# Performance work log

Hardware: AMD Instinct MI355X
Metric: run time of the kernel (lower is better)

The kernel has to match this reference:

```python
import jax, jax.numpy as jnp
import numpy as np

B, S, W = 128, 100, 20
D, L, H, DFF = 192, 6, 8, 256
DH = D // H

def _ln(x, g, b, eps=1e-5):
    m = jnp.mean(x, -1, keepdims=True)
    v = jnp.var(x, -1, keepdims=True)
    return (x - m) * jax.lax.rsqrt(v + eps) * g + b

def _pos_encoding(seq_len, d):
    pos = np.arange(seq_len, dtype=np.float32)[:, None]
    div = np.exp(np.arange(0, d, 2, dtype=np.float32) * (-np.log(10000.0) / d))
    pe = np.zeros((seq_len, d), dtype=np.float32)
    pe[:, 0::2] = np.sin(pos * div)
    pe[:, 1::2] = np.cos(pos * div)
    return jnp.asarray(pe)

def setup_inputs() -> dict:
    key = jax.random.key(0)
    ks = iter(jax.random.split(key, 80))
    def nrm(shape, s=0.05):
        return jax.random.normal(next(ks), shape, jnp.float32) * s
    inp = {
        'title_idx': jax.random.randint(next(ks), (B, S, W), 0, 1000),
        'class_idx': jax.random.randint(next(ks), (B, S, W), 0, 500),
        'process_idx': jax.random.randint(next(ks), (B, S, W), 0, 1000),
        'activity_type': jax.random.randint(next(ks), (B, S), 0, 4),
        'mouse_pos': jax.random.uniform(next(ks), (B, S, 2), jnp.float32),
        'rect': jax.random.uniform(next(ks), (B, S, W, 4), jnp.float32),
        'flags': jax.random.uniform(next(ks), (B, S, W, 2), jnp.float32),
        'keyboard_active': jax.random.uniform(next(ks), (B, S, 1), jnp.float32),
        'window_mask': jnp.ones((B, S, W), jnp.float32),
        'noise': jax.random.normal(next(ks), (W, B, D), jnp.float32),
        'title_emb': nrm((1000, 32)),
        'class_emb': nrm((500, 32)),
        'process_emb': nrm((1000, 32)),
        'spatial_w1': nrm((64, 6)), 'spatial_b1': nrm((64,)),
        'spatial_w2': nrm((32, 64)), 'spatial_b2': nrm((32,)),
        'wfuse_w': nrm((128, 128)), 'wfuse_b': nrm((128,)),
        'mouse_w1': nrm((32, 2)), 'mouse_b1': nrm((32,)),
        'mouse_w2': nrm((32, 32)), 'mouse_b2': nrm((32,)),
        'act_emb': nrm((4, 16)),
        'kbd_w': nrm((16, 1)), 'kbd_b': nrm((16,)),
        'afuse_w': nrm((64, 64)), 'afuse_b': nrm((64,)),
        'qkv_w': nrm((L, 3 * D, D)), 'qkv_b': nrm((L, 3 * D)),
        'out_w': nrm((L, D, D)), 'out_b': nrm((L, D)),
        'ff1_w': nrm((L, DFF, D)), 'ff1_b': nrm((L, DFF)),
        'ff2_w': nrm((L, D, DFF)), 'ff2_b': nrm((L, D)),
        'ln1_g': 1.0 + nrm((L, D)), 'ln1_b': nrm((L, D)),
        'ln2_g': 1.0 + nrm((L, D)), 'ln2_b': nrm((L, D)),
        'proj_w1': nrm((256, 192)), 'proj_b1': nrm((256,)),
        'proj_w2': nrm((4, 256)), 'proj_b2': nrm((4,)),
        'ex_w1': nrm((128, 192)), 'ex_b1': nrm((128,)),
        'ex_w2': nrm((1, 128)), 'ex_b2': nrm((1,)),
    }
    return inp

def reference(title_idx, class_idx, process_idx, activity_type, mouse_pos, rect, flags, keyboard_active, window_mask, noise, title_emb, class_emb, process_emb, spatial_w1, spatial_b1, spatial_w2, spatial_b2, wfuse_w, wfuse_b, mouse_w1, mouse_b1, mouse_w2, mouse_b2, act_emb, kbd_w, kbd_b, afuse_w, afuse_b, qkv_w, qkv_b, out_w, out_b, ff1_w, ff1_b, ff2_w, ff2_b, ln1_g, ln1_b, ln2_g, ln2_b, proj_w1, proj_b1, proj_w2, proj_b2, ex_w1, ex_b1, ex_w2, ex_b2):
    # ---- window feature extraction (vectorized over B,S,W) ----
    t = title_emb[title_idx]              # [B,S,W,32]
    c = class_emb[class_idx]
    p = process_emb[process_idx]
    sp_in = jnp.concatenate([rect, flags], -1)  # [B,S,W,6]
    sp = jax.nn.relu(sp_in @ spatial_w1.T + spatial_b1) @ spatial_w2.T + spatial_b2
    wcomb = jnp.concatenate([t, c, p, sp], -1)  # [B,S,W,128]
    wf = jax.nn.relu(wcomb @ wfuse_w.T + wfuse_b) * window_mask[..., None]
    avg_w = jnp.sum(wf, 2) / W            # mean over max_windows incl zero padding
    # ---- activity feature extraction ----
    mp = mouse_pos / jnp.array([1920.0, 1080.0], jnp.float32)
    mf = jax.nn.relu(mp @ mouse_w1.T + mouse_b1) @ mouse_w2.T + mouse_b2  # [B,S,32]
    ae = act_emb[activity_type]           # [B,S,16]
    kf = keyboard_active @ kbd_w.T + kbd_b  # [B,S,16]
    af = jax.nn.relu(jnp.concatenate([mf, ae, kf], -1) @ afuse_w.T + afuse_b)
    # ---- transformer ----
    x = jnp.concatenate([avg_w, af], -1) + _pos_encoding(S, D)[None]  # [B,S,192]
    scale = 1.0 / np.sqrt(DH)
    def block(h, prm):
        qw, qb, ow, ob, f1w, f1b, f2w, f2b, g1, b1, g2, b2 = prm
        qkv = h @ qw.T + qb
        q, k, v = jnp.split(qkv, 3, -1)
        q = q.reshape(B, S, H, DH); k = k.reshape(B, S, H, DH); v = v.reshape(B, S, H, DH)
        a = jax.nn.softmax(jnp.einsum('bqhd,bkhd->bhqk', q, k) * scale, -1)
        o = jnp.einsum('bhqk,bkhd->bqhd', a, v).reshape(B, S, D)
        h = _ln(h + o @ ow.T + ob, g1, b1)
        ff = jax.nn.relu(h @ f1w.T + f1b) @ f2w.T + f2b
        return _ln(h + ff, g2, b2), None
    x, _ = jax.lax.scan(block, x, (qkv_w, qkv_b, out_w, out_b, ff1_w, ff1_b, ff2_w, ff2_b, ln1_g, ln1_b, ln2_g, ln2_b))
    last = x[:, -1, :]                    # [B,192]
    # ---- per-slot heads (noise passed in deterministically) ----
    slot = last[None] + noise * 0.1       # [W,B,192]
    positions = jnp.transpose(jax.nn.relu(slot @ proj_w1.T + proj_b1) @ proj_w2.T + proj_b2, (1, 0, 2))  # [B,W,4]
    existence = jnp.transpose(jax.nn.sigmoid(jax.nn.relu(slot @ ex_w1.T + ex_b1) @ ex_w2.T + ex_b2)[..., 0], (1, 0))  # [B,W]
    return positions, existence
```

## Files before the change

### kernel.cpp

```cpp
#include <hip/hip_runtime.h>
#include <hip/hip_bf16.h>
#include <math.h>

#define B_ 128
#define S_ 100
#define W_ 20
#define D_ 192
#define L_ 6
#define H_ 8
#define DFF_ 256
#define DH_ 24
#define BS_ (B_*S_)
#define THREED_ 576

typedef short short8 __attribute__((ext_vector_type(8)));
typedef short short4v __attribute__((ext_vector_type(4)));
typedef float floatx16 __attribute__((ext_vector_type(16)));

__device__ __forceinline__ float posenc(int s, int c) {
  float freq = expf(-logf(10000.f) * (float)(2 * (c >> 1)) / (float)D_);
  float ang = (float)s * freq;
  return (c & 1) ? cosf(ang) : sinf(ang);
}

__device__ __forceinline__ short8 ld_frag8(const __hip_bfloat16* p) {
  short4v lo = *(const short4v*)p;
  short4v hi = *(const short4v*)(p + 4);
  short8 r;
  r[0]=lo[0]; r[1]=lo[1]; r[2]=lo[2]; r[3]=lo[3];
  r[4]=hi[0]; r[5]=hi[1]; r[6]=hi[2]; r[7]=hi[3];
  return r;
}

__device__ __forceinline__ short f2bf_s(float v) {
  __hip_bfloat16 t = __float2bfloat16(v);
  return *reinterpret_cast<short*>(&t);
}

__global__ __launch_bounds__(256)
void convertprep_kernel(
    const float* __restrict__ s0, __hip_bfloat16* __restrict__ d0,
    const float* __restrict__ s1, __hip_bfloat16* __restrict__ d1,
    const float* __restrict__ s2, __hip_bfloat16* __restrict__ d2,
    const float* __restrict__ s3, __hip_bfloat16* __restrict__ d3,
    const float* __restrict__ te, const float* __restrict__ ce,
    const float* __restrict__ pe, const float* __restrict__ wfw,
    const float* __restrict__ wfb, const float* __restrict__ sw2,
    const float* __restrict__ sb2,
    float* __restrict__ TE2, float* __restrict__ CE2,
    float* __restrict__ PE2, __hip_bfloat16* __restrict__ WSPb)
{
  int b = blockIdx.x, tid = threadIdx.x;
  if (b < 720) {
    const float* s; __hip_bfloat16* d; int base;
    if      (b < 324) { s = s0; d = d0; base = b; }
    else if (b < 432) { s = s1; d = d1; base = b - 324; }
    else if (b < 576) { s = s2; d = d2; base = b - 432; }
    else              { s = s3; d = d3; base = b - 576; }
    int i = (base * 256 + tid) * 8;
    float4 v0 = *(const float4*)(s + i);
    float4 v1 = *(const float4*)(s + i + 4);
    __hip_bfloat162* d2p = (__hip_bfloat162*)(d + i);
    d2p[0] = __float22bfloat162_rn(make_float2(v0.x, v0.y));
    d2p[1] = __float22bfloat162_rn(make_float2(v0.z, v0.w));
    d2p[2] = __float22bfloat162_rn(make_float2(v1.x, v1.y));
    d2p[3] = __float22bfloat162_rn(make_float2(v1.z, v1.w));
    return;
  }
  int blk = b - 720;
  if (blk < 1250) {
    int item = blk * 256 + tid;
    int v = item >> 7, o = item & 127;
    const float* src; float* dst; int base, vv;
    float a;
    if (v < 1000) {
      src = te; dst = TE2; base = 0; vv = v;
      a = wfb[o];
      #pragma unroll 8
      for (int k = 0; k < 32; ++k) a += wfw[o * 128 + 96 + k] * sb2[k];
    } else if (v < 1500) {
      src = ce; dst = CE2; base = 32; vv = v - 1000; a = 0.f;
    } else {
      src = pe; dst = PE2; base = 64; vv = v - 1500; a = 0.f;
    }
    #pragma unroll 8
    for (int k = 0; k < 32; ++k) a += src[vv * 32 + k] * wfw[o * 128 + base + k];
    dst[vv * 128 + o] = a;
  } else {
    int item = (blk - 1250) * 256 + tid;
    int j = item >> 7, o = item & 127;
    float a = 0.f;
    #pragma unroll 8
    for (int k = 0; k < 32; ++k) a += wfw[o * 128 + 96 + k] * sw2[k * 64 + j];
    WSPb[o * 64 + j] = __float2bfloat16(a);
  }
}

__global__ __launch_bounds__(256)
void encode8_kernel(
    const int* __restrict__ title_idx, const int* __restrict__ class_idx,
    const int* __restrict__ process_idx, const int* __restrict__ activity_type,
    const float* __restrict__ mouse_pos, const float* __restrict__ rect,
    const float* __restrict__ flags, const float* __restrict__ keyboard_active,
    const float* __restrict__ window_mask,
    const float* __restrict__ sw1, const float* __restrict__ sb1,
    const float* __restrict__ TE2, const float* __restrict__ CE2,
    const float* __restrict__ PE2, const __hip_bfloat16* __restrict__ WSPb,
    const float* __restrict__ mw1, const float* __restrict__ mb1,
    const float* __restrict__ mw2, const float* __restrict__ mb2,
    const float* __restrict__ act_emb, const float* __restrict__ kbw,
    const float* __restrict__ kbb,
    const float* __restrict__ afw, const float* __restrict__ afb,
    float* __restrict__ x, __hip_bfloat16* __restrict__ xb)
{
  __shared__ __hip_bfloat16 Bls[128][72];
  __shared__ int   idxS[4][20][3];
  __shared__ float maskS[4][20];
  __shared__ __align__(16) char aux[2560];
  float (*rectS)[20][8] = (float(*)[20][8])aux;
  float (*afA)[68]      = (float(*)[68])aux;
  float (*afB)[68]      = (float(*)[68])(aux + 1088);

  int tid = threadIdx.x;
  int w = tid >> 6, lane = tid & 63;
  int m32 = lane & 31, half = lane >> 5;
  int bs0 = blockIdx.x * 4;
  int bs = bs0 + w;

  for (int e = tid; e < 240; e += 256) {
    int g2 = e / 60, rem = e % 60, which = rem / 20, w_ = rem % 20;
    const int* src = (which == 0) ? title_idx : (which == 1) ? class_idx : process_idx;
    idxS[g2][w_][which] = src[(bs0 + g2) * W_ + w_];
  }
  if (tid < 80) {
    int g2 = tid / 20, w_ = tid % 20;
    maskS[g2][w_] = window_mask[(bs0 + g2) * W_ + w_];
  }
  for (int e = tid; e < 480; e += 256) {
    int g2 = e / 120, rem = e % 120, w_ = rem / 6, c = rem % 6;
    int rg = (bs0 + g2) * W_ + w_;
    rectS[g2][w_][c] = (c < 4) ? rect[rg * 4 + c] : flags[rg * 2 + (c - 4)];
  }
  for (int e = tid; e < 1024; e += 256) {
    int col = e >> 3, k8 = e & 7;
    short8 v = *(const short8*)&WSPb[col * 64 + k8 * 8];
    *(short8*)&Bls[col][k8 * 8] = v;
  }
  __syncthreads();

  short8 afr[4];
  {
    float rc[6];
    bool act = (m32 < W_);
    if (act) {
      #pragma unroll
      for (int c = 0; c < 6; ++c) rc[c] = rectS[w][m32][c];
    }
    #pragma unroll
    for (int s = 0; s < 4; ++s) {
      short8 f;
      #pragma unroll
      for (int jp = 0; jp < 8; ++jp) {
        float a = 0.f;
        if (act) {
          int j = s * 16 + half * 8 + jp;
          const float* w1 = sw1 + j * 6;
          a = sb1[j];
          #pragma unroll
          for (int c = 0; c < 6; ++c) a += w1[c] * rc[c];
          a = fmaxf(a, 0.f);
        }
        f[jp] = f2bf_s(a);
      }
      afr[s] = f;
    }
  }

  floatx16 acc[4];
  #pragma unroll
  for (int nt = 0; nt < 4; ++nt)
    #pragma unroll
    for (int r = 0; r < 16; ++r) acc[nt][r] = 0.f;

  #pragma unroll
  for (int s = 0; s < 4; ++s) {
    int ko = s * 16 + half * 8;
    #pragma unroll
    for (int nt = 0; nt < 4; ++nt) {
      short8 bf = *(const short8*)&Bls[nt * 32 + m32][ko];
      acc[nt] = __builtin_amdgcn_mfma_f32_32x32x16_bf16(afr[s], bf, acc[nt], 0, 0, 0);
    }
  }

  float cs[4] = {0.f, 0.f, 0.f, 0.f};
  #pragma unroll
  for (int r = 0; r < 16; ++r) {
    int row = (r & 3) + 8 * (r >> 2) + 4 * half;
    if (row < W_) {
      int t  = idxS[w][row][0];
      int ci = idxS[w][row][1];
      int p  = idxS[w][row][2];
      float mk = maskS[w][row];
      #pragma unroll
      for (int nt = 0; nt < 4; ++nt) {
        int col = nt * 32 + m32;
        float gs = TE2[(size_t)t  * 128 + col]
                 + CE2[(size_t)ci * 128 + col]
                 + PE2[(size_t)p  * 128 + col];
        cs[nt] += fmaxf(acc[nt][r] + gs, 0.f) * mk;
      }
    }
  }
  #pragma unroll
  for (int nt = 0; nt < 4; ++nt) cs[nt] += __shfl_xor(cs[nt], 32);
  if (half == 0) {
    int s_ = bs % S_;
    #pragma unroll
    for (int nt = 0; nt < 4; ++nt) {
      int col = nt * 32 + m32;
      float v = cs[nt] * (1.f / (float)W_) + posenc(s_, col);
      x[(size_t)bs * D_ + col] = v;
      xb[(size_t)bs * D_ + col] = __float2bfloat16(v);
    }
  }

  int bl = tid >> 6, ln63 = tid & 63;
  int bsg = bs0 + bl;
  __syncthreads();
  if (ln63 < 32) {
    float mx = mouse_pos[bsg * 2 + 0] * (1.f / 1920.f);
    float my = mouse_pos[bsg * 2 + 1] * (1.f / 1080.f);
    afA[bl][ln63] = fmaxf(mw1[ln63 * 2] * mx + mw1[ln63 * 2 + 1] * my + mb1[ln63], 0.f);
  }
  __syncthreads();
  float cv;
  if (ln63 < 32) {
    float a = mb2[ln63];
    #pragma unroll 8
    for (int k = 0; k < 32; ++k) a += mw2[ln63 * 32 + k] * afA[bl][k];
    cv = a;
  } else if (ln63 < 48) {
    cv = act_emb[activity_type[bsg] * 16 + (ln63 - 32)];
  } else {
    cv = kbw[ln63 - 48] * keyboard_active[bsg] + kbb[ln63 - 48];
  }
  __syncthreads();
  afB[bl][ln63] = cv;
  __syncthreads();
  {
    float a = afb[ln63];
    const float4* w4 = (const float4*)(afw + ln63 * 64);
    const float4* cp = (const float4*)&afB[bl][0];
    #pragma unroll
    for (int k4 = 0; k4 < 16; ++k4) {
      float4 ww = w4[k4], c2 = cp[k4];
      a += ww.x*c2.x + ww.y*c2.y + ww.z*c2.z + ww.w*c2.w;
    }
    float v = fmaxf(a, 0.f);
    int cg = 128 + ln63;
    float ovv = v + posenc(bsg % S_, cg);
    x[(size_t)bsg * D_ + cg] = ovv;
    xb[(size_t)bsg * D_ + cg] = __float2bfloat16(ovv);
  }
}

__global__ __launch_bounds__(256)
void qkvattn_kernel(const __hip_bfloat16* __restrict__ xb,
                    const __hip_bfloat16* __restrict__ Wq,
                    const float* __restrict__ qb,
                    __hip_bfloat16* __restrict__ o)
{
  __shared__ __align__(16) char smem[40960];
  __hip_bfloat16* Asl = (__hip_bfloat16*)smem;
  __hip_bfloat16* Bsl = (__hip_bfloat16*)(smem + 10240);
  __hip_bfloat16* Qs  = (__hip_bfloat16*)smem;
  __hip_bfloat16* Ks  = (__hip_bfloat16*)(smem + 10240);
  __hip_bfloat16* Ps  = (__hip_bfloat16*)smem;
  __hip_bfloat16* Vt  = (__hip_bfloat16*)(smem + 33792);

  int bh = blockIdx.x;
  int hh = bh & 7, b = bh >> 3;
  int tid = threadIdx.x, lane = tid & 63, w = tid >> 6;
  int m32 = lane & 31, half = lane >> 5;

  for (int e = tid; e < (32 * 112) / 8; e += 256)
    ((float4*)Vt)[e] = make_float4(0.f, 0.f, 0.f, 0.f);

  int rA = tid >> 1, hA = tid & 1;
  int rrA = rA < S_ ? rA : S_ - 1;
  size_t baseA = (size_t)(b * S_ + rrA) * D_;
  float4* dA = (float4*)&Asl[rA * 40 + hA * 16];

  bool isB = (tid < 192);
  int rB = tid >> 1;
  int tB = rB >> 5, jB = rB & 31;
  bool actB = isB && (jB < DH_);
  size_t baseB = actB ? (size_t)(tB * D_ + hh * DH_ + jB) * D_ : 0;
  float4* dB = (float4*)&Bsl[rB * 40 + hA * 16];

  if (isB && !actB) {
    float4 z = make_float4(0.f, 0.f, 0.f, 0.f);
    dB[0] = z; dB[1] = z;
  }
  {
    float4 a0, a1, b0, b1;
    const float4* s = (const float4*)&xb[baseA + hA * 16];
    a0 = s[0]; a1 = s[1];
    if (actB) {
      const float4* sB = (const float4*)&Wq[baseB + hA * 16];
      b0 = sB[0]; b1 = sB[1];
      dB[0] = b0; dB[1] = b1;
    }
    dA[0] = a0; dA[1] = a1;
  }

  floatx16 acc[3];
  #pragma unroll
  for (int t = 0; t < 3; ++t)
    #pragma unroll
    for (int r = 0; r < 16; ++r) acc[t][r] = 0.f;

  for (int k0 = 0; k0 < D_; k0 += 32) {
    bool more = (k0 + 32 < D_);
    __syncthreads();
    float4 na0, na1, nb0, nb1;
    if (more) {
      const float4* s = (const float4*)&xb[baseA + k0 + 32 + hA * 16];
      na0 = s[0]; na1 = s[1];
      if (actB) {
        const float4* sB = (const float4*)&Wq[baseB + k0 + 32 + hA * 16];
        nb0 = sB[0]; nb1 = sB[1];
      }
    }
    #pragma unroll
    for (int kc = 0; kc < 2; ++kc) {
      int ko = kc * 16 + half * 8;
      short8 a = *(const short8*)&Asl[(w * 32 + m32) * 40 + ko];
      #pragma unroll
      for (int t = 0; t < 3; ++t) {
        short8 bf = *(const short8*)&Bsl[(t * 32 + m32) * 40 + ko];
        acc[t] = __builtin_amdgcn_mfma_f32_32x32x16_bf16(a, bf, acc[t], 0, 0, 0);
      }
    }
    __syncthreads();
    if (more) {
      dA[0] = na0; dA[1] = na1;
      if (actB) { dB[0] = nb0; dB[1] = nb1; }
    }
  }
  {
    bool dv = (m32 < DH_);
    float bq = dv ? qb[0 * D_ + hh * DH_ + m32] : 0.f;
    float bk = dv ? qb[1 * D_ + hh * DH_ + m32] : 0.f;
    float bv = dv ? qb[2 * D_ + hh * DH_ + m32] : 0.f;
    #pragma unroll
    for (int r = 0; r < 16; ++r) {
      int row = w * 32 + (r & 3) + 8 * (r >> 2) + 4 * half;
      Qs[row * 40 + m32] = __float2bfloat16(dv ? acc[0][r] + bq : 0.f);
      Ks[row * 40 + m32] = __float2bfloat16(dv ? acc[1][r] + bk : 0.f);
      if (dv && row < S_) Vt[m32 * 112 + row] = __float2bfloat16(acc[2][r] + bv);
    }
  }
  __syncthreads();

  floatx16 sc[4];
  #pragma unroll
  for (int nt = 0; nt < 4; ++nt)
    #pragma unroll
    for (int r = 0; r < 16; ++r) sc[nt][r] = 0.f;
  #pragma unroll
  for (int kc = 0; kc < 2; ++kc) {
    int ko = kc * 16 + half * 8;
    short8 a = *(const short8*)&Qs[(w * 32 + m32) * 40 + ko];
    #pragma unroll
    for (int nt = 0; nt < 4; ++nt) {
      short8 bf = *(const short8*)&Ks[(nt * 32 + m32) * 40 + ko];
      sc[nt] = __builtin_amdgcn_mfma_f32_32x32x16_bf16(a, bf, sc[nt], 0, 0, 0);
    }
  }
  __syncthreads();

  const float scale = 0.20412414523193154f;
  float rinv[16];
  #pragma unroll
  for (int r = 0; r < 16; ++r) {
    float mx = -1e30f;
    #pragma unroll
    for (int nt = 0; nt < 4; ++nt) {
      float s = sc[nt][r] * scale;
      if (nt == 3 && m32 >= 4) s = -1e30f;
      sc[nt][r] = s;
      mx = fmaxf(mx, s);
    }
    #pragma unroll
    for (int off = 1; off < 32; off <<= 1) mx = fmaxf(mx, __shfl_xor(mx, off));
    float sum = 0.f;
    #pragma unroll
    for (int nt = 0; nt < 4; ++nt) {
      float e = expf(sc[nt][r] - mx);
      sc[nt][r] = e;
      sum += e;
    }
    #pragma unroll
    for (int off = 1; off < 32; off <<= 1) sum += __shfl_xor(sum, off);
    rinv[r] = 1.f / sum;
  }
  #pragma unroll
  for (int r = 0; r < 16; ++r) {
    int rowl = (r & 3) + 8 * (r >> 2) + 4 * half;
    #pragma unroll
    for (int nt = 0; nt < 4; ++nt)
      Ps[(w * 32 + rowl) * 132 + nt * 32 + m32] = __float2bfloat16(sc[nt][r]);
  }

  floatx16 ov;
  #pragma unroll
  for (int r = 0; r < 16; ++r) ov[r] = 0.f;
  #pragma unroll
  for (int kt = 0; kt < 7; ++kt) {
    int ko = kt * 16 + half * 8;
    short8 a = ld_frag8(&Ps[(w * 32 + m32) * 132 + ko]);
    short8 bf = *(const short8*)&Vt[m32 * 112 + ko];
    ov = __builtin_amdgcn_mfma_f32_32x32x16_bf16(a, bf, ov, 0, 0, 0);
  }
  #pragma unroll
  for (int r = 0; r < 16; ++r) {
    int rowl = (r & 3) + 8 * (r >> 2) + 4 * half;
    int q = w * 32 + rowl;
    if (m32 < DH_ && q < S_)
      o[((size_t)(b * S_ + q)) * D_ + hh * DH_ + m32] =
          __float2bfloat16(ov[r] * rinv[r]);
  }
}

__global__ __launch_bounds__(256)
void outffln_kernel(const __hip_bfloat16* __restrict__ attb,
                    const __hip_bfloat16* __restrict__ Wo, const float* __restrict__ bo,
                    const float* __restrict__ g1, const float* __restrict__ b1v,
                    const __hip_bfloat16* __restrict__ W1, const float* __restrict__ b1,
                    const __hip_bfloat16* __restrict__ W2, const float* __restrict__ b2,
                    const float* __restrict__ g2, const float* __restrict__ b2v,
                    float* __restrict__ x, __hip_bfloat16* __restrict__ xb)
{
  __shared__ __align__(16) char arena[59904];
  __hip_bfloat16* AslA = (__hip_bfloat16*)arena;
  __hip_bfloat16* BslA = (__hip_bfloat16*)(arena + 5120);
  __hip_bfloat16* C1   = (__hip_bfloat16*)arena;
  __hip_bfloat16* AslB = (__hip_bfloat16*)(arena + 33280);
  __hip_bfloat16* BslB = (__hip_bfloat16*)(arena + 38400);
  float (*psum)[2] = (float(*)[2])(arena + 58880);
  float (*psq)[2]  = (float(*)[2])(arena + 59392);

  int tid = threadIdx.x, lane = tid & 63, w = tid >> 6;
  int m32 = lane & 31, half = lane >> 5;
  int mt = w & 1, ng = w >> 1;
  int bm = blockIdx.x * 64;

  floatx16 accA[3];
  #pragma unroll
  for (int j = 0; j < 3; ++j)
    #pragma unroll
    for (int r = 0; r < 16; ++r) accA[j][r] = 0.f;

  for (int k0 = 0; k0 < D_; k0 += 32) {
    if (tid < 128) {
      int r = tid >> 1, h = tid & 1;
      const float4* s = (const float4*)(attb + (size_t)(bm + r) * D_ + k0 + h * 16);
      float4* d = (float4*)&AslA[r * 40 + h * 16];
      d[0] = s[0]; d[1] = s[1];
    }
    for (int e = tid; e < 384; e += 256) {
      int r = e >> 1, h = e & 1;
      const float4* s = (const float4*)(Wo + (size_t)r * D_ + k0 + h * 16);
      float4* d = (float4*)&BslA[r * 40 + h * 16];
      d[0] = s[0]; d[1] = s[1];
    }
    __syncthreads();
    #pragma unroll
    for (int kc = 0; kc < 2; ++kc) {
      int ko = kc * 16 + half * 8;
      short8 a = *(const short8*)&AslA[(mt * 32 + m32) * 40 + ko];
      #pragma unroll
      for (int j = 0; j < 3; ++j) {
        short8 bf = *(const short8*)&BslA[((ng * 3 + j) * 32 + m32) * 40 + ko];
        accA[j] = __builtin_amdgcn_mfma_f32_32x32x16_bf16(a, bf, accA[j], 0, 0, 0);
      }
    }
    __syncthreads();
  }
  {
    int rowb = mt * 32 + 4 * half;
    #pragma unroll
    for (int r = 0; r < 16; ++r) {
      int rl = rowb + (r & 3) + 8 * (r >> 2);
      int row = bm + rl;
      float p = 0.f;
      #pragma unroll
      for (int j = 0; j < 3; ++j) {
        int col = (ng * 3 + j) * 32 + m32;
        float t = accA[j][r] + bo[col] + x[(size_t)row * D_ + col];
        accA[j][r] = t;
        p += t;
      }
      #pragma unroll
      for (int off = 1; off < 32; off <<= 1) p += __shfl_xor(p, off);
      if (m32 == 0) psum[rl][ng] = p;
    }
    __syncthreads();
    float mean[16];
    #pragma unroll
    for (int r = 0; r < 16; ++r) {
      int rl = rowb + (r & 3) + 8 * (r >> 2);
      mean[r] = (psum[rl][0] + psum[rl][1]) * (1.f / (float)D_);
    }
    #pragma unroll
    for (int r = 0; r < 16; ++r) {
      int rl = rowb + (r & 3) + 8 * (r >> 2);
      float s = 0.f;
      #pragma unroll
      for (int j = 0; j < 3; ++j) { float dd = accA[j][r] - mean[r]; s += dd * dd; }
      #pragma unroll
      for (int off = 1; off < 32; off <<= 1) s += __shfl_xor(s, off);
      if (m32 == 0) psq[rl][ng] = s;
    }
    __syncthreads();
    #pragma unroll
    for (int r = 0; r < 16; ++r) {
      int rl = rowb + (r & 3) + 8 * (r >> 2);
      int row = bm + rl;
      float inv = rsqrtf((psq[rl][0] + psq[rl][1]) * (1.f / (float)D_) + 1e-5f);
      #pragma unroll
      for (int j = 0; j < 3; ++j) {
        int col = (ng * 3 + j) * 32 + m32;
        float ovv = (accA[j][r] - mean[r]) * inv * g1[col] + b1v[col];
        x[(size_t)row * D_ + col] = ovv;
        xb[(size_t)row * D_ + col] = __float2bfloat16(ovv);
      }
    }
  }
  __syncthreads();

  floatx16 acc1[4];
  #pragma unroll
  for (int j = 0; j < 4; ++j)
    #pragma unroll
    for (int r = 0; r < 16; ++r) acc1[j][r] = 0.f;

  for (int k0 = 0; k0 < D_; k0 += 32) {
    if (tid < 128) {
      int r = tid >> 1, h = tid & 1;
      const float4* s = (const float4*)(xb + (size_t)(bm + r) * D_ + k0 + h * 16);
      float4* d = (float4*)&AslB[r * 40 + h * 16];
      d[0] = s[0]; d[1] = s[1];
    }
    for (int e = tid; e < 512; e += 256) {
      int r = e >> 1, h = e & 1;
      const float4* s = (const float4*)(W1 + (size_t)r * D_ + k0 + h * 16);
      float4* d = (float4*)&BslB[r * 40 + h * 16];
      d[0] = s[0]; d[1] = s[1];
    }
    __syncthreads();
    #pragma unroll
    for (int kc = 0; kc < 2; ++kc) {
      int ko = kc * 16 + half * 8;
      short8 a = *(const short8*)&AslB[(mt * 32 + m32) * 40 + ko];
      #pragma unroll
      for (int j = 0; j < 4; ++j) {
        short8 bf = *(const short8*)&BslB[((ng * 4 + j) * 32 + m32) * 40 + ko];
        acc1[j] = __builtin_amdgcn_mfma_f32_32x32x16_bf16(a, bf, acc1[j], 0, 0, 0);
      }
    }
    __syncthreads();
  }
  {
    int rowb = mt * 32 + 4 * half;
    #pragma unroll
    for (int j = 0; j < 4; ++j) {
      int col = (ng * 4 + j) * 32 + m32;
      float cb = b1[col];
      #pragma unroll
      for (int r = 0; r < 16; ++r) {
        int row = rowb + (r & 3) + 8 * (r >> 2);
        C1[row * 260 + col] = __float2bfloat16(fmaxf(acc1[j][r] + cb, 0.f));
      }
    }
  }
  __syncthreads();

  floatx16 acc2[3];
  #pragma unroll
  for (int j = 0; j < 3; ++j)
    #pragma unroll
    for (int r = 0; r < 16; ++r) acc2[j][r] = 0.f;

  for (int k0 = 0; k0 < DFF_; k0 += 32) {
    for (int e = tid; e < 384; e += 256) {
      int r = e >> 1, h = e & 1;
      const float4* s = (const float4*)(W2 + (size_t)r * DFF_ + k0 + h * 16);
      float4* d = (float4*)&BslB[r * 40 + h * 16];
      d[0] = s[0]; d[1] = s[1];
    }
    __syncthreads();
    #pragma unroll
    for (int kc = 0; kc < 2; ++kc) {
      int ko = kc * 16 + half * 8;
      short8 a = ld_frag8(&C1[(mt * 32 + m32) * 260 + k0 + ko]);
      #pragma unroll
      for (int j = 0; j < 3; ++j) {
        short8 bf = *(const short8*)&BslB[((ng * 3 + j) * 32 + m32) * 40 + ko];
        acc2[j] = __builtin_amdgcn_mfma_f32_32x32x16_bf16(a, bf, acc2[j], 0, 0, 0);
      }
    }
    __syncthreads();
  }

  int rowb = mt * 32 + 4 * half;
  #pragma unroll
  for (int r = 0; r < 16; ++r) {
    int rl = rowb + (r & 3) + 8 * (r >> 2);
    int row = bm + rl;
    float p = 0.f;
    #pragma unroll
    for (int j = 0; j < 3; ++j) {
      int col = (ng * 3 + j) * 32 + m32;
      float t = acc2[j][r] + b2[col] + x[(size_t)row * D_ + col];
      acc2[j][r] = t;
      p += t;
    }
    #pragma unroll
    for (int off = 1; off < 32; off <<= 1) p += __shfl_xor(p, off);
    if (m32 == 0) psum[rl][ng] = p;
  }
  __syncthreads();
  float mean[16];
  #pragma unroll
  for (int r = 0; r < 16; ++r) {
    int rl = rowb + (r & 3) + 8 * (r >> 2);
    mean[r] = (psum[rl][0] + psum[rl][1]) * (1.f / (float)D_);
  }
  #pragma unroll
  for (int r = 0; r < 16; ++r) {
    int rl = rowb + (r & 3) + 8 * (r >> 2);
    float s = 0.f;
    #pragma unroll
    for (int j = 0; j < 3; ++j) { float dd = acc2[j][r] - mean[r]; s += dd * dd; }
    #pragma unroll
    for (int off = 1; off < 32; off <<= 1) s += __shfl_xor(s, off);
    if (m32 == 0) psq[rl][ng] = s;
  }
  __syncthreads();
  #pragma unroll
  for (int r = 0; r < 16; ++r) {
    int rl = rowb + (r & 3) + 8 * (r >> 2);
    int row = bm + rl;
    float inv = rsqrtf((psq[rl][0] + psq[rl][1]) * (1.f / (float)D_) + 1e-5f);
    #pragma unroll
    for (int j = 0; j < 3; ++j) {
      int col = (ng * 3 + j) * 32 + m32;
      float ovv = (acc2[j][r] - mean[r]) * inv * g2[col] + b2v[col];
      x[(size_t)row * D_ + col] = ovv;
      xb[(size_t)row * D_ + col] = __float2bfloat16(ovv);
    }
  }
}

__global__ __launch_bounds__(256)
void head2_kernel(const float* __restrict__ x, const float* __restrict__ noise,
                  const float* __restrict__ pw1, const float* __restrict__ pb1,
                  const float* __restrict__ pw2, const float* __restrict__ pb2,
                  const float* __restrict__ ew1, const float* __restrict__ eb1,
                  const float* __restrict__ ew2, const float* __restrict__ eb2,
                  float* __restrict__ out)
{
  __shared__ float slotS[20][192];
  __shared__ float phS[20][256];
  __shared__ float ehS[20][128];
  int b = blockIdx.x;
  int tid = threadIdx.x;

  const float* lastrow = x + ((size_t)b * S_ + (S_ - 1)) * D_;
  for (int e = tid; e < 20 * 192; e += 256) {
    int w = e / 192, c = e - w * 192;
    slotS[w][c] = lastrow[c] + noise[((size_t)w * B_ + b) * D_ + c] * 0.1f;
  }
  __syncthreads();

  bool doe = (tid < 128);
  float accp[20], acce[20];
  {
    float bp = pb1[tid];
    float be = doe ? eb1[tid] : 0.f;
    #pragma unroll
    for (int w = 0; w < 20; ++w) { accp[w] = bp; acce[w] = be; }
  }
  {
    const float4* wr = (const float4*)(pw1 + (size_t)tid * D_);
    const float4* we = (const float4*)(ew1 + (size_t)(doe ? tid : 0) * D_);
    for (int k4 = 0; k4 < 48; ++k4) {
      float4 wv = wr[k4];
      float4 ev = we[k4];
      #pragma unroll
      for (int w = 0; w < 20; ++w) {
        float4 sv = *(const float4*)&slotS[w][k4 * 4];
        accp[w] += wv.x*sv.x + wv.y*sv.y + wv.z*sv.z + wv.w*sv.w;
        if (doe) acce[w] += ev.x*sv.x + ev.y*sv.y + ev.z*sv.z + ev.w*sv.w;
      }
    }
  }
  #pragma unroll
  for (int w = 0; w < 20; ++w) {
    phS[w][tid] = fmaxf(accp[w], 0.f);
    if (doe) ehS[w][tid] = fmaxf(acce[w], 0.f);
  }
  __syncthreads();

  if (tid < 80) {
    int w = tid >> 2, c = tid & 3;
    float a = pb2[c];
    const float4* wr = (const float4*)(pw2 + c * 256);
    const float4* pp = (const float4*)&phS[w][0];
    for (int k = 0; k < 64; ++k) {
      float4 wv = wr[k], pv = pp[k];
      a += wv.x*pv.x + wv.y*pv.y + wv.z*pv.z + wv.w*pv.w;
    }
    out[((size_t)b * W_ + w) * 4 + c] = a;
  } else if (tid < 100) {
    int w = tid - 80;
    float a = eb2[0];
    const float4* wr = (const float4*)ew2;
    const float4* pp = (const float4*)&ehS[w][0];
    for (int k = 0; k < 32; ++k) {
      float4 wv = wr[k], pv = pp[k];
      a += wv.x*pv.x + wv.y*pv.y + wv.z*pv.z + wv.w*pv.w;
    }
    out[(size_t)B_ * W_ * 4 + (size_t)b * W_ + w] = 1.f / (1.f + expf(-a));
  }
}

extern "C" void kernel_launch(void* const* d_in, const int* in_sizes, int n_in,
                              void* d_out, int out_size, void* d_ws, size_t ws_size,
                              hipStream_t stream)
{
  const int*   title_idx       = (const int*)  d_in[0];
  const int*   class_idx       = (const int*)  d_in[1];
  const int*   process_idx     = (const int*)  d_in[2];
  const int*   activity_type   = (const int*)  d_in[3];
  const float* mouse_pos       = (const float*)d_in[4];
  const float* rect            = (const float*)d_in[5];
  const float* flags           = (const float*)d_in[6];
  const float* keyboard_active = (const float*)d_in[7];
  const float* window_mask     = (const float*)d_in[8];
  const float* noise           = (const float*)d_in[9];
  const float* title_emb       = (const float*)d_in[10];
  const float* class_emb       = (const float*)d_in[11];
  const float* process_emb     = (const float*)d_in[12];
  const float* spatial_w1      = (const float*)d_in[13];
  const float* spatial_b1      = (const float*)d_in[14];
  const float* spatial_w2      = (const float*)d_in[15];
  const float* spatial_b2      = (const float*)d_in[16];
  const float* wfuse_w         = (const float*)d_in[17];
  const float* wfuse_b         = (const float*)d_in[18];
  const float* mouse_w1        = (const float*)d_in[19];
  const float* mouse_b1        = (const float*)d_in[20];
  const float* mouse_w2        = (const float*)d_in[21];
  const float* mouse_b2        = (const float*)d_in[22];
  const float* act_emb         = (const float*)d_in[23];
  const float* kbd_w           = (const float*)d_in[24];
  const float* kbd_b           = (const float*)d_in[25];
  const float* afuse_w         = (const float*)d_in[26];
  const float* afuse_b         = (const float*)d_in[27];
  const float* qkv_w           = (const float*)d_in[28];
  const float* qkv_b           = (const float*)d_in[29];
  const float* out_w           = (const float*)d_in[30];
  const float* out_b           = (const float*)d_in[31];
  const float* ff1_w           = (const float*)d_in[32];
  const float* ff1_b           = (const float*)d_in[33];
  const float* ff2_w           = (const float*)d_in[34];
  const float* ff2_b           = (const float*)d_in[35];
  const float* ln1_g           = (const float*)d_in[36];
  const float* ln1_b           = (const float*)d_in[37];
  const float* ln2_g           = (const float*)d_in[38];
  const float* ln2_b           = (const float*)d_in[39];
  const float* proj_w1         = (const float*)d_in[40];
  const float* proj_b1         = (const float*)d_in[41];
  const float* proj_w2         = (const float*)d_in[42];
  const float* proj_b2         = (const float*)d_in[43];
  const float* ex_w1           = (const float*)d_in[44];
  const float* ex_b1           = (const float*)d_in[45];
  const float* ex_w2           = (const float*)d_in[46];
  const float* ex_b2           = (const float*)d_in[47];

  float* out = (float*)d_out;

  float* x = (float*)d_ws;
  __hip_bfloat16* xb   = (__hip_bfloat16*)(x + (size_t)BS_ * D_);
  __hip_bfloat16* attb = xb   + (size_t)BS_ * D_;
  __hip_bfloat16* wqb  = attb + (size_t)BS_ * D_;
  __hip_bfloat16* wob  = wqb  + (size_t)L_ * THREED_ * D_;
  __hip_bfloat16* wf1b = wob  + (size_t)L_ * D_ * D_;
  __hip_bfloat16* wf2b = wf1b + (size_t)L_ * DFF_ * D_;
  float* TE2  = (float*)(wf2b + (size_t)L_ * D_ * DFF_);
  float* CE2  = TE2  + 1000 * 128;
  float* PE2  = CE2  + 500 * 128;
  __hip_bfloat16* WSPb = (__hip_bfloat16*)(PE2 + 1000 * 128);
  (void)ws_size; (void)n_in; (void)in_sizes; (void)out_size;

  convertprep_kernel<<<2002, 256, 0, stream>>>(
      qkv_w, wqb, out_w, wob, ff1_w, wf1b, ff2_w, wf2b,
      title_emb, class_emb, process_emb, wfuse_w, wfuse_b,
      spatial_w2, spatial_b2, TE2, CE2, PE2, WSPb);

  encode8_kernel<<<BS_ / 4, 256, 0, stream>>>(
      title_idx, class_idx, process_idx, activity_type, mouse_pos, rect, flags,
      keyboard_active, window_mask, spatial_w1, spatial_b1,
      TE2, CE2, PE2, WSPb,
      mouse_w1, mouse_b1, mouse_w2, mouse_b2, act_emb, kbd_w, kbd_b,
      afuse_w, afuse_b, x, xb);

  for (int l = 0; l < L_; ++l) {
    qkvattn_kernel<<<B_ * H_, 256, 0, stream>>>(
        xb, wqb + (size_t)l * THREED_ * D_, qkv_b + (size_t)l * THREED_, attb);
    outffln_kernel<<<BS_ / 64, 256, 0, stream>>>(
        attb, wob + (size_t)l * D_ * D_, out_b + (size_t)l * D_,
        ln1_g + (size_t)l * D_, ln1_b + (size_t)l * D_,
        wf1b + (size_t)l * DFF_ * D_, ff1_b + (size_t)l * DFF_,
        wf2b + (size_t)l * D_ * DFF_, ff2_b + (size_t)l * D_,
        ln2_g + (size_t)l * D_, ln2_b + (size_t)l * D_, x, xb);
  }

  head2_kernel<<<B_, 256, 0, stream>>>(
      x, noise, proj_w1, proj_b1, proj_w2, proj_b2,
      ex_w1, ex_b1, ex_w2, ex_b2, out);
}
```

Measured before the change: 745.8 us.

## Register-prefetch next K-tile in fused out-proj/FFN GEMM loops

The three K-loops of the fused attention-output/FFN kernel now load the next K-slice of activations and weights into registers before the MFMA work on the current slice, then write them to shared memory after the barrier. This overlaps global memory latency with compute, replacing the load-sync-compute-sync pattern. The convertprep kernel also switches its scalar dot-product loops to float4 loads. The change costs more registers, which may lower occupancy. The barrier after the C1 write was removed; correctness now relies on the first barrier inside the next loop, and C1 shares the arena with AslA, not with BslB.

```diff
diff --git a/kernel.cpp b/kernel.cpp
--- a/kernel.cpp
+++ b/kernel.cpp
@@ -35,6 +35,10 @@
 __device__ __forceinline__ short f2bf_s(float v) {
   __hip_bfloat16 t = __float2bfloat16(v);
   return *reinterpret_cast<short*>(&t);
+}
+
+__device__ __forceinline__ float dot4(float4 a, float4 b) {
+  return a.x*b.x + a.y*b.y + a.z*b.z + a.w*b.w;
 }
 
 __global__ __launch_bounds__(256)
@@ -76,15 +80,19 @@
     if (v < 1000) {
       src = te; dst = TE2; base = 0; vv = v;
       a = wfb[o];
-      #pragma unroll 8
-      for (int k = 0; k < 32; ++k) a += wfw[o * 128 + 96 + k] * sb2[k];
+      const float4* w4 = (const float4*)(wfw + o * 128 + 96);
+      const float4* b4 = (const float4*)sb2;
+      #pragma unroll
+      for (int k4 = 0; k4 < 8; ++k4) a += dot4(w4[k4], b4[k4]);
     } else if (v < 1500) {
       src = ce; dst = CE2; base = 32; vv = v - 1000; a = 0.f;
     } else {
       src = pe; dst = PE2; base = 64; vv = v - 1500; a = 0.f;
     }
-    #pragma unroll 8
-    for (int k = 0; k < 32; ++k) a += src[vv * 32 + k] * wfw[o * 128 + base + k];
+    const float4* s4 = (const float4*)(src + vv * 32);
+    const float4* w4 = (const float4*)(wfw + o * 128 + base);
+    #pragma unroll
+    for (int k4 = 0; k4 < 8; ++k4) a += dot4(s4[k4], w4[k4]);
     dst[vv * 128 + o] = a;
   } else {
     int item = (blk - 1250) * 256 + tid;
@@ -456,37 +464,72 @@
   int mt = w & 1, ng = w >> 1;
   int bm = blockIdx.x * 64;
 
+  bool sA = (tid < 128);
+  int rA = tid >> 1, hA = tid & 1;
+  int r0 = tid >> 1, h0 = tid & 1;
+  int r1 = (tid + 256) >> 1, h1 = tid & 1;
+
   floatx16 accA[3];
   #pragma unroll
   for (int j = 0; j < 3; ++j)
     #pragma unroll
     for (int r = 0; r < 16; ++r) accA[j][r] = 0.f;
 
-  for (int k0 = 0; k0 < D_; k0 += 32) {
-    if (tid < 128) {
-      int r = tid >> 1, h = tid & 1;
-      const float4* s = (const float4*)(attb + (size_t)(bm + r) * D_ + k0 + h * 16);
-      float4* d = (float4*)&AslA[r * 40 + h * 16];
-      d[0] = s[0]; d[1] = s[1];
-    }
-    for (int e = tid; e < 384; e += 256) {
-      int r = e >> 1, h = e & 1;
-      const float4* s = (const float4*)(Wo + (size_t)r * D_ + k0 + h * 16);
-      float4* d = (float4*)&BslA[r * 40 + h * 16];
-      d[0] = s[0]; d[1] = s[1];
-    }
-    __syncthreads();
-    #pragma unroll
-    for (int kc = 0; kc < 2; ++kc) {
-      int ko = kc * 16 + half * 8;
-      short8 a = *(const short8*)&AslA[(mt * 32 + m32) * 40 + ko];
-      #pragma unroll
-      for (int j = 0; j < 3; ++j) {
-        short8 bf = *(const short8*)&BslA[((ng * 3 + j) * 32 + m32) * 40 + ko];
-        accA[j] = __builtin_amdgcn_mfma_f32_32x32x16_bf16(a, bf, accA[j], 0, 0, 0);
-      }
-    }
-    __syncthreads();
+  {
+    float4* dA  = (float4*)&AslA[rA * 40 + hA * 16];
+    float4* dB0 = (float4*)&BslA[r0 * 40 + h0 * 16];
+    float4* dB1 = (float4*)&BslA[r1 * 40 + h1 * 16];
+    bool s1 = (tid < 128);
+
+    {
+      if (sA) {
+        const float4* s = (const float4*)(attb + (size_t)(bm + rA) * D_ + hA * 16);
+        dA[0] = s[0]; dA[1] = s[1];
+      }
+      {
+        const float4* s = (const float4*)(Wo + (size_t)r0 * D_ + h0 * 16);
+        dB0[0] = s[0]; dB0[1] = s[1];
+      }
+      if (s1) {
+        const float4* s = (const float4*)(Wo + (size_t)r1 * D_ + h1 * 16);
+        dB1[0] = s[0]; dB1[1] = s[1];
+      }
+    }
+    for (int k0 = 0; k0 < D_; k0 += 32) {
+      bool more = (k0 + 32 < D_);
+      __syncthreads();
+      float4 na0, na1, nb00, nb01, nb10, nb11;
+      if (more) {
+        if (sA) {
+          const float4* s = (const float4*)(attb + (size_t)(bm + rA) * D_ + k0 + 32 + hA * 16);
+          na0 = s[0]; na1 = s[1];
+        }
+        {
+          const float4* s = (const float4*)(Wo + (size_t)r0 * D_ + k0 + 32 + h0 * 16);
+          nb00 = s[0]; nb01 = s[1];
+        }
+        if (s1) {
+          const float4* s = (const float4*)(Wo + (size_t)r1 * D_ + k0 + 32 + h1 * 16);
+          nb10 = s[0]; nb11 = s[1];
+        }
+      }
+      #pragma unroll
+      for (int kc = 0; kc < 2; ++kc) {
+        int ko = kc * 16 + half * 8;
+        short8 a = *(const short8*)&AslA[(mt * 32 + m32) * 40 + ko];
+        #pragma unroll
+        for (int j = 0; j < 3; ++j) {
+          short8 bf = *(const short8*)&BslA[((ng * 3 + j) * 32 + m32) * 40 + ko];
+          accA[j] = __builtin_amdgcn_mfma_f32_32x32x16_bf16(a, bf, accA[j], 0, 0, 0);
+        }
+      }
+      __syncthreads();
+      if (more) {
+        if (sA) { dA[0] = na0; dA[1] = na1; }
+        dB0[0] = nb00; dB0[1] = nb01;
+        if (s1) { dB1[0] = nb10; dB1[1] = nb11; }
+      }
+    }
   }
   {
     int rowb = mt * 32 + 4 * half;
@@ -546,31 +589,60 @@
     #pragma unroll
     for (int r = 0; r < 16; ++r) acc1[j][r] = 0.f;
 
-  for (int k0 = 0; k0 < D_; k0 += 32) {
-    if (tid < 128) {
-      int r = tid >> 1, h = tid & 1;
-      const float4* s = (const float4*)(xb + (size_t)(bm + r) * D_ + k0 + h * 16);
-      float4* d = (float4*)&AslB[r * 40 + h * 16];
-      d[0] = s[0]; d[1] = s[1];
-    }
-    for (int e = tid; e < 512; e += 256) {
-      int r = e >> 1, h = e & 1;
-      const float4* s = (const float4*)(W1 + (size_t)r * D_ + k0 + h * 16);
-      float4* d = (float4*)&BslB[r * 40 + h * 16];
-      d[0] = s[0]; d[1] = s[1];
-    }
-    __syncthreads();
-    #pragma unroll
-    for (int kc = 0; kc < 2; ++kc) {
-      int ko = kc * 16 + half * 8;
-      short8 a = *(const short8*)&AslB[(mt * 32 + m32) * 40 + ko];
-      #pragma unroll
-      for (int j = 0; j < 4; ++j) {
-        short8 bf = *(const short8*)&BslB[((ng * 4 + j) * 32 + m32) * 40 + ko];
-        acc1[j] = __builtin_amdgcn_mfma_f32_32x32x16_bf16(a, bf, acc1[j], 0, 0, 0);
-      }
-    }
-    __syncthreads();
+  {
+    float4* dA  = (float4*)&AslB[rA * 40 + hA * 16];
+    float4* dB0 = (float4*)&BslB[r0 * 40 + h0 * 16];
+    float4* dB1 = (float4*)&BslB[r1 * 40 + h1 * 16];
+
+    {
+      if (sA) {
+        const float4* s = (const float4*)(xb + (size_t)(bm + rA) * D_ + hA * 16);
+        dA[0] = s[0]; dA[1] = s[1];
+      }
+      {
+        const float4* s = (const float4*)(W1 + (size_t)r0 * D_ + h0 * 16);
+        dB0[0] = s[0]; dB0[1] = s[1];
+      }
+      {
+        const float4* s = (const float4*)(W1 + (size_t)r1 * D_ + h1 * 16);
+        dB1[0] = s[0]; dB1[1] = s[1];
+      }
+    }
+    for (int k0 = 0; k0 < D_; k0 += 32) {
+      bool more = (k0 + 32 < D_);
+      __syncthreads();
+      float4 na0, na1, nb00, nb01, nb10, nb11;
+      if (more) {
+        if (sA) {
+          const float4* s = (const float4*)(xb + (size_t)(bm + rA) * D_ + k0 + 32 + hA * 16);
+          na0 = s[0]; na1 = s[1];
+        }
+        {
+          const float4* s = (const float4*)(W1 + (size_t)r0 * D_ + k0 + 32 + h0 * 16);
+          nb00 = s[0]; nb01 = s[1];
+        }
+        {
+          const float4* s = (const float4*)(W1 + (size_t)r1 * D_ + k0 + 32 + h1 * 16);
+          nb10 = s[0]; nb11 = s[1];
+        }
+      }
+      #pragma unroll
+      for (int kc = 0; kc < 2; ++kc) {
+        int ko = kc * 16 + half * 8;
+        short8 a = *(const short8*)&AslB[(mt * 32 + m32) * 40 + ko];
+        #pragma unroll
+        for (int j = 0; j < 4; ++j) {
+          short8 bf = *(const short8*)&BslB[((ng * 4 + j) * 32 + m32) * 40 + ko];
+          acc1[j] = __builtin_amdgcn_mfma_f32_32x32x16_bf16(a, bf, acc1[j], 0, 0, 0);
+        }
+      }
+      __syncthreads();
+      if (more) {
+        if (sA) { dA[0] = na0; dA[1] = na1; }
+        dB0[0] = nb00; dB0[1] = nb01;
+        dB1[0] = nb10; dB1[1] = nb11;
+      }
+    }
   }
   {
     int rowb = mt * 32 + 4 * half;
@@ -585,7 +657,6 @@
       }
     }
   }
-  __syncthreads();
 
   floatx16 acc2[3];
   #pragma unroll
@@ -593,25 +664,49 @@
     #pragma unroll
     for (int r = 0; r < 16; ++r) acc2[j][r] = 0.f;
 
-  for (int k0 = 0; k0 < DFF_; k0 += 32) {
-    for (int e = tid; e < 384; e += 256) {
-      int r = e >> 1, h = e & 1;
-      const float4* s = (const float4*)(W2 + (size_t)r * DFF_ + k0 + h * 16);
-      float4* d = (float4*)&BslB[r * 40 + h * 16];
-      d[0] = s[0]; d[1] = s[1];
-    }
-    __syncthreads();
-    #pragma unroll
-    for (int kc = 0; kc < 2; ++kc) {
-      int ko = kc * 16 + half * 8;
-      short8 a = ld_frag8(&C1[(mt * 32 + m32) * 260 + k0 + ko]);
-      #pragma unroll
-      for (int j = 0; j < 3; ++j) {
-        short8 bf = *(const short8*)&BslB[((ng * 3 + j) * 32 + m32) * 40 + ko];
-        acc2[j] = __builtin_amdgcn_mfma_f32_32x32x16_bf16(a, bf, acc2[j], 0, 0, 0);
-      }
-    }
-    __syncthreads();
+  {
+    float4* dB0 = (float4*)&BslB[r0 * 40 + h0 * 16];
+    float4* dB1 = (float4*)&BslB[r1 * 40 + h1 * 16];
+    bool s1 = (tid < 128);
+
+    {
+      const float4* s = (const float4*)(W2 + (size_t)r0 * DFF_ + h0 * 16);
+      dB0[0] = s[0]; dB0[1] = s[1];
+      if (s1) {
+        const float4* s2 = (const float4*)(W2 + (size_t)r1 * DFF_ + h1 * 16);
+        dB1[0] = s2[0]; dB1[1] = s2[1];
+      }
+    }
+    for (int k0 = 0; k0 < DFF_; k0 += 32) {
+      bool more = (k0 + 32 < DFF_);
+      __syncthreads();
+      float4 nb00, nb01, nb10, nb11;
+      if (more) {
+        {
+          const float4* s = (const float4*)(W2 + (size_t)r0 * DFF_ + k0 + 32 + h0 * 16);
+          nb00 = s[0]; nb01 = s[1];
+        }
+        if (s1) {
+          const float4* s = (const float4*)(W2 + (size_t)r1 * DFF_ + k0 + 32 + h1 * 16);
+          nb10 = s[0]; nb11 = s[1];
+        }
+      }
+      #pragma unroll
+      for (int kc = 0; kc < 2; ++kc) {
+        int ko = kc * 16 + half * 8;
+        short8 a = ld_frag8(&C1[(mt * 32 + m32) * 260 + k0 + ko]);
+        #pragma unroll
+        for (int j = 0; j < 3; ++j) {
+          short8 bf = *(const short8*)&BslB[((ng * 3 + j) * 32 + m32) * 40 + ko];
+          acc2[j] = __builtin_amdgcn_mfma_f32_32x32x16_bf16(a, bf, acc2[j], 0, 0, 0);
+        }
+      }
+      __syncthreads();
+      if (more) {
+        dB0[0] = nb00; dB0[1] = nb01;
+        if (s1) { dB1[0] = nb10; dB1[1] = nb11; }
+      }
+    }
   }
 
   int rowb = mt * 32 + 4 * half;
```

Measured after the change: 724.0 us. 2.9% less time.
